# Optimization experiments

Hardware: AMD Instinct MI355X
Metric: run time of the kernel (lower is better)

The kernel has to match this reference:

```python
import jax, jax.numpy as jnp
import numpy as np

NEG_SLOPE = 0.2
NUM_NODES = 100000
NUM_EDGES = 200000
NNZ = 1600000
IN_C = 128
OUT_C = 128
STAR = 64


def setup_inputs() -> dict:
    key = jax.random.key(0)
    ks = jax.random.split(key, 12)
    X = jax.random.normal(ks[0], (NUM_NODES, IN_C), dtype=jnp.float32)
    V = jax.random.randint(ks[1], (NNZ,), 0, NUM_NODES)
    E = jax.random.randint(ks[2], (NNZ,), 0, NUM_EDGES)
    S_features = jax.random.normal(ks[3], (NUM_EDGES, STAR), dtype=jnp.float32)
    s = 1.0 / np.sqrt(IN_C)
    Wx = jax.random.uniform(ks[4], (IN_C, OUT_C), minval=-s, maxval=s)
    bx = jax.random.uniform(ks[5], (OUT_C,), minval=-s, maxval=s)
    Wv = jax.random.uniform(ks[6], (IN_C, OUT_C), minval=-s, maxval=s)
    bv = jax.random.uniform(ks[7], (OUT_C,), minval=-s, maxval=s)
    sa = 1.0 / np.sqrt(OUT_C)
    a_vec = jax.random.uniform(ks[8], (OUT_C,), minval=-sa, maxval=sa)
    st = 1.0 / np.sqrt(OUT_C + STAR)
    Wt = jax.random.uniform(ks[9], (OUT_C + STAR, OUT_C), minval=-st, maxval=st)
    bt = jax.random.uniform(ks[10], (OUT_C,), minval=-st, maxval=st)
    return {"X": X, "V": V, "E": E, "S_features": S_features,
            "Wx": Wx, "bx": bx, "Wv": Wv, "bv": bv,
            "a_vec": a_vec, "Wt": Wt, "bt": bt}


def _segment_softmax(s, seg, num_segments):
    m = jax.ops.segment_max(s, seg, num_segments=num_segments)
    e = jnp.exp(s - m[seg])
    denom = jax.ops.segment_sum(e, seg, num_segments=num_segments)
    return e / denom[seg]


def reference(X, V, E, S_features, Wx, bx, Wv, bv, a_vec, Wt, bt):
    # DPHGNNConv forward (eval mode: dropout = identity)
    X_init = X @ Wx + bx                      # [N, out]
    X_feat = X @ Wv + bv                      # [N, out]
    scores = X_feat @ a_vec                   # [N]
    s = jax.nn.leaky_relu(scores[V], NEG_SLOPE)  # [nnz]
    w = _segment_softmax(s, E, NUM_EDGES)     # [nnz]
    Xev = X_feat[V] * w[:, None]              # [nnz, out]
    Y_v2e = jax.ops.segment_sum(Xev, E, num_segments=NUM_EDGES)
    Y_v2e = jax.nn.elu(Y_v2e)
    e_msg = jnp.concatenate([Y_v2e, S_features], axis=1)  # [E, out+star]
    Y = e_msg @ Wt + bt                       # [E, out]
    Yev = Y[E]                                # [nnz, out]
    num = jax.ops.segment_sum(Yev, V, num_segments=NUM_NODES)
    cnt = jax.ops.segment_sum(jnp.ones((NNZ,), jnp.float32), V, num_segments=NUM_NODES)
    Xn = num / jnp.maximum(cnt, 1.0)[:, None]  # scatter_mean
    Xn = jax.nn.elu(Xn)                        # is_last=False
    return Xn + X_init
```

## Files before the change

kernel.cpp:

```cpp
#include <hip/hip_runtime.h>
#include <math.h>

#define N_NODES 100000
#define N_EDGES 200000
#define NNZ_    1600000
#define INC  128
#define OUTC 128
#define STAR_ 64
#define NEG 0.2f
#define MAXE 32
#define MAXN 64
#define NBIN_E 391
#define NBIN_V 196
#define NBIN (NBIN_E + NBIN_V)
#define CHUNK 4000

typedef __attribute__((ext_vector_type(8))) short bf16x8_t;
typedef __attribute__((ext_vector_type(4))) float f32x4_t;

__device__ __forceinline__ float leaky(float x){ return x > 0.f ? x : NEG*x; }
__device__ __forceinline__ float elu1(float x){ return x > 0.f ? x : __expf(x)-1.f; }
__device__ __forceinline__ unsigned short f2bf(float f){
  unsigned u = __float_as_uint(f);
  unsigned r = u + 0x7FFFu + ((u >> 16) & 1u);
  return (unsigned short)(r >> 16);
}
__device__ __forceinline__ float bf2f(unsigned short h){
  return __uint_as_float(((unsigned)h) << 16);
}

__global__ void k_cvt(const float* __restrict__ Wx, const float* __restrict__ Wv,
                      const float* __restrict__ Wt,
                      unsigned short* __restrict__ WcatT, unsigned short* __restrict__ WtT){
  const int i = blockIdx.x*256 + threadIdx.x;
  if (i < 256*128){
    const int n = i >> 7, k = i & 127;
    const float v = (n < 128) ? Wx[k*128 + n] : Wv[k*128 + (n-128)];
    WcatT[n*128 + k] = f2bf(v);
  }
  const int j = i - 256*128;
  if (j >= 0 && j < 128*192){
    const int n = j / 192, k = j - n*192;
    WtT[n*192 + k] = f2bf(Wt[k*128 + n]);
  }
}

__global__ __launch_bounds__(256) void k_gemm1(const float* __restrict__ X,
    const unsigned short* __restrict__ WcatT,
    const float* __restrict__ bx, const float* __restrict__ bv,
    float* __restrict__ Xinit, unsigned short* __restrict__ Xfb){
  __shared__ unsigned short xb[16][136];
  const int tid = threadIdx.x;
  const int lane = tid & 63, w = tid >> 6;
  const int quad = lane >> 4, l16 = lane & 15;
  const int r0 = blockIdx.x * 16;
  {
    const int r = tid >> 4;
    const int c0 = (tid & 15) * 8;
    const float4 a4 = *(const float4*)&X[(size_t)(r0+r)*INC + c0];
    const float4 b4 = *(const float4*)&X[(size_t)(r0+r)*INC + c0 + 4];
    bf16x8_t pk;
    pk[0]=(short)f2bf(a4.x); pk[1]=(short)f2bf(a4.y); pk[2]=(short)f2bf(a4.z); pk[3]=(short)f2bf(a4.w);
    pk[4]=(short)f2bf(b4.x); pk[5]=(short)f2bf(b4.y); pk[6]=(short)f2bf(b4.z); pk[7]=(short)f2bf(b4.w);
    *(bf16x8_t*)&xb[r][c0] = pk;
  }
  __syncthreads();
  f32x4_t acc[4] = {{0,0,0,0},{0,0,0,0},{0,0,0,0},{0,0,0,0}};
  const int n_base = w*64 + l16;
  for (int s = 0; s < 4; ++s){
    const bf16x8_t af = *(const bf16x8_t*)&xb[l16][s*32 + quad*8];
    #pragma unroll
    for (int nt = 0; nt < 4; ++nt){
      const int n = n_base + nt*16;
      const bf16x8_t bf = *(const bf16x8_t*)&WcatT[(size_t)n*128 + s*32 + quad*8];
      acc[nt] = __builtin_amdgcn_mfma_f32_16x16x32_bf16(af, bf, acc[nt], 0, 0, 0);
    }
  }
  #pragma unroll
  for (int nt = 0; nt < 4; ++nt){
    const int n = n_base + nt*16;
    const float bias = (n < 128) ? bx[n] : bv[n-128];
    #pragma unroll
    for (int r = 0; r < 4; ++r){
      const int m = quad*4 + r;
      const float val = acc[nt][r] + bias;
      if (n < 128) Xinit[(size_t)(r0+m)*OUTC + n] = val;
      else         Xfb[(size_t)(r0+m)*OUTC + (n-128)] = f2bf(val);
    }
  }
}

__global__ __launch_bounds__(256) void k_scores(const unsigned short* __restrict__ Xfb,
    const float* __restrict__ a, float* __restrict__ scores){
  const int lane = threadIdx.x & 63;
  const int w = threadIdx.x >> 6;
  const int r = blockIdx.x * 4 + w;
  const unsigned pair = *(const unsigned*)&Xfb[(size_t)r*OUTC + lane*2];
  float p = bf2f((unsigned short)(pair & 0xffff)) * a[lane*2]
          + bf2f((unsigned short)(pair >> 16))    * a[lane*2+1];
  #pragma unroll
  for (int o = 32; o; o >>= 1) p += __shfl_xor(p, o, 64);
  if (lane == 0) scores[r] = p;
}


__global__ __launch_bounds__(256) void k_binhist(const int* __restrict__ V, const int* __restrict__ E,
                                                 int* __restrict__ binCnt){
  __shared__ int h[NBIN];
  for (int p = threadIdx.x; p < NBIN; p += 256) h[p] = 0;
  __syncthreads();
  const int start = blockIdx.x*CHUNK, end = start + CHUNK;
  for (int i = start + threadIdx.x; i < end; i += 256){
    atomicAdd(&h[E[i] >> 9], 1);
    atomicAdd(&h[NBIN_E + (V[i] >> 9)], 1);
  }
  __syncthreads();
  for (int p = threadIdx.x; p < NBIN; p += 256) if (h[p]) atomicAdd(&binCnt[p], h[p]);
}

__global__ __launch_bounds__(1024) void k_binscan(const int* __restrict__ binCnt,
                                                  int* __restrict__ binBase, int* __restrict__ binCur){
  __shared__ int s[1024];
  const int tid = threadIdx.x;
  const int v = (tid < NBIN) ? binCnt[tid] : 0;
  s[tid] = v; __syncthreads();
  for (int o = 1; o < 1024; o <<= 1){
    const int u = (tid >= o) ? s[tid-o] : 0;
    __syncthreads();
    s[tid] += u;
    __syncthreads();
  }
  if (tid < NBIN){ binBase[tid] = s[tid] - v; binCur[tid] = s[tid] - v; }
}

__global__ __launch_bounds__(256) void k_binA(const int* __restrict__ V, const int* __restrict__ E,
                                              int* __restrict__ binCur, int2* __restrict__ pair){
  __shared__ int h[NBIN];
  __shared__ int base[NBIN];
  for (int p = threadIdx.x; p < NBIN; p += 256) h[p] = 0;
  __syncthreads();
  const int start = blockIdx.x*CHUNK, end = start + CHUNK;
  for (int i = start + threadIdx.x; i < end; i += 256){
    atomicAdd(&h[E[i] >> 9], 1);
    atomicAdd(&h[NBIN_E + (V[i] >> 9)], 1);
  }
  __syncthreads();
  for (int p = threadIdx.x; p < NBIN; p += 256)
    base[p] = h[p] ? atomicAdd(&binCur[p], h[p]) : 0;
  __syncthreads();
  for (int p = threadIdx.x; p < NBIN; p += 256) h[p] = 0;
  __syncthreads();
  for (int i = start + threadIdx.x; i < end; i += 256){
    const int e = E[i], v = V[i];
    const int be = e >> 9, bv = NBIN_E + (v >> 9);
    const int se = base[be] + atomicAdd(&h[be], 1);
    const int sv = base[bv] + atomicAdd(&h[bv], 1);
    pair[se] = make_int2(e, v);
    pair[sv] = make_int2(v, e);
  }
}

__global__ __launch_bounds__(256) void k_binB(const int2* __restrict__ pair,
    const int* __restrict__ binBase, const int* __restrict__ binCnt,
    int* __restrict__ vIdxE, int* __restrict__ eIdxV,
    int* __restrict__ cntE, int* __restrict__ startsE,
    int* __restrict__ cntV, int* __restrict__ startsV){
  __shared__ int h[512], sc0[512], sc1[512];
  const int bin = blockIdx.x;
  const bool isE = bin < NBIN_E;
  const int nb = isE ? bin : bin - NBIN_E;
  const int bucket0 = nb << 9;
  const int nBuckTot = isE ? N_EDGES : N_NODES;
  const int start = binBase[bin];
  const int n = binCnt[bin];
  const int itemBase = isE ? start : start - NNZ_;
  const int tid = threadIdx.x;
  for (int p = tid; p < 512; p += 256) h[p] = 0;
  __syncthreads();
  for (int j = tid; j < n; j += 256) atomicAdd(&h[pair[start + j].x & 511], 1);
  __syncthreads();
  for (int p = tid; p < 512; p += 256) sc0[p] = h[p];
  __syncthreads();
  int* a = sc0; int* b = sc1;
  for (int o = 1; o < 512; o <<= 1){
    for (int p = tid; p < 512; p += 256) b[p] = a[p] + (p >= o ? a[p-o] : 0);
    __syncthreads();
    int* t = a; a = b; b = t;
  }
  for (int p = tid; p < 512; p += 256){
    const int excl = a[p] - h[p];
    b[p] = itemBase + excl;
    const int bucket = bucket0 + p;
    if (bucket < nBuckTot){
      if (isE){ cntE[bucket] = h[p]; startsE[bucket] = itemBase + excl; }
      else    { cntV[bucket] = h[p]; startsV[bucket] = itemBase + excl; }
    }
  }
  __syncthreads();
  for (int j = tid; j < n; j += 256){
    const int2 kv = pair[start + j];
    const int slot = atomicAdd(&b[kv.x & 511], 1);
    if (isE) vIdxE[slot] = kv.y; else eIdxV[slot] = kv.y;
  }
}

__global__ __launch_bounds__(256) void k_edge(
    const int* __restrict__ cntE, const int* __restrict__ startsE,
    const int* __restrict__ vIdxE,
    const float* __restrict__ scores, const unsigned short* __restrict__ Xfb,
    const float* __restrict__ S, const unsigned short* __restrict__ WtT,
    const float* __restrict__ bt, unsigned short* __restrict__ Ybf) {
  __shared__ int   wvs[16][MAXE];
  __shared__ float wws[16][MAXE];
  __shared__ unsigned short msg[16][200];
  __shared__ float ms[16], dens[16];
  __shared__ int   degs[16], sts[16];
  const int tid = threadIdx.x;
  const int lane = tid & 63, w = tid >> 6;
  const int e0 = blockIdx.x * 16;

  for (int p = tid; p < 16*MAXE; p += 256) { ((int*)wvs)[p] = 0; ((float*)wws)[p] = 0.f; }
  __syncthreads();

  for (int q = 0; q < 4; ++q) {
    const int t = w*4 + q;
    const int e = e0 + t;
    const int deg = cntE[e], st = startsE[e];
    if (deg <= 64) {
      int v = 0; float ls = -INFINITY;
      if (lane < deg) { v = vIdxE[st + lane]; ls = leaky(scores[v]); }
      float m = ls;
      #pragma unroll
      for (int o = 32; o; o >>= 1) m = fmaxf(m, __shfl_xor(m, o, 64));
      const float ex = (lane < deg) ? __expf(ls - m) : 0.f;
      float dsum = ex;
      #pragma unroll
      for (int o = 32; o; o >>= 1) dsum += __shfl_xor(dsum, o, 64);
      if (lane < deg && lane < MAXE) { wvs[t][lane] = v; wws[t][lane] = ex; }
      if (lane == 0) { ms[t] = m; dens[t] = dsum; degs[t] = deg; sts[t] = st; }
    } else {
      float m = -INFINITY;
      for (int j = lane; j < deg; j += 64)
        m = fmaxf(m, leaky(scores[vIdxE[st + j]]));
      #pragma unroll
      for (int o = 32; o; o >>= 1) m = fmaxf(m, __shfl_xor(m, o, 64));
      float dsum = 0.f;
      for (int j = lane; j < deg; j += 64) {
        const int v = vIdxE[st + j];
        const float ex = __expf(leaky(scores[v]) - m);
        dsum += ex;
        if (j < MAXE) { wvs[t][j] = v; wws[t][j] = ex; }
      }
      #pragma unroll
      for (int o = 32; o; o >>= 1) dsum += __shfl_xor(dsum, o, 64);
      if (lane == 0) { ms[t] = m; dens[t] = dsum; degs[t] = deg; sts[t] = st; }
    }
  }
  __syncthreads();

  const int sub = tid & 31, grp = tid >> 5;
  const int c4 = sub * 4;
  if (sub < 16) {
    const int cs = sub * 4;
    #pragma unroll
    for (int tt = 0; tt < 2; ++tt) {
      const int t = grp*2 + tt;
      const float4 s4 = *(const float4*)&S[(size_t)(e0+t)*STAR_ + cs];
      ushort4 pk; pk.x=f2bf(s4.x); pk.y=f2bf(s4.y); pk.z=f2bf(s4.z); pk.w=f2bf(s4.w);
      *(ushort4*)&msg[t][128 + cs] = pk;
    }
  }
  #pragma unroll
  for (int tt = 0; tt < 2; ++tt) {
    const int t = grp*2 + tt;
    const int deg = degs[t];
    const int dc = deg < MAXE ? deg : MAXE;
    const int dc4 = (dc + 3) & ~3;
    float a0=0.f, a1=0.f, a2=0.f, a3=0.f;
    for (int j = 0; j < dc4; j += 4) {
      #pragma unroll
      for (int ii = 0; ii < 4; ++ii) {
        const int v = wvs[t][j+ii];
        const float wgt = wws[t][j+ii];
        const ushort4 x = *(const ushort4*)&Xfb[(size_t)v*OUTC + c4];
        a0 += wgt * bf2f(x.x); a1 += wgt * bf2f(x.y);
        a2 += wgt * bf2f(x.z); a3 += wgt * bf2f(x.w);
      }
    }
    for (int j = MAXE; j < deg; ++j) {
      const int v = vIdxE[sts[t] + j];
      const float wgt = __expf(leaky(scores[v]) - ms[t]);
      const ushort4 x = *(const ushort4*)&Xfb[(size_t)v*OUTC + c4];
      a0 += wgt * bf2f(x.x); a1 += wgt * bf2f(x.y);
      a2 += wgt * bf2f(x.z); a3 += wgt * bf2f(x.w);
    }
    const float invd = deg > 0 ? 1.f/dens[t] : 0.f;
    ushort4 pk;
    pk.x = f2bf(elu1(a0*invd)); pk.y = f2bf(elu1(a1*invd));
    pk.z = f2bf(elu1(a2*invd)); pk.w = f2bf(elu1(a3*invd));
    *(ushort4*)&msg[t][c4] = pk;
  }
  __syncthreads();

  const int quad = lane >> 4, l16 = lane & 15;
  f32x4_t acc0 = {0,0,0,0}, acc1 = {0,0,0,0};
  const int n0 = w * 32;
  for (int s = 0; s < 6; ++s) {
    const bf16x8_t af = *(const bf16x8_t*)&msg[l16][s*32 + quad*8];
    const bf16x8_t b0 = *(const bf16x8_t*)&WtT[(size_t)(n0 + l16)*192      + s*32 + quad*8];
    const bf16x8_t b1 = *(const bf16x8_t*)&WtT[(size_t)(n0 + 16 + l16)*192 + s*32 + quad*8];
    acc0 = __builtin_amdgcn_mfma_f32_16x16x32_bf16(af, b0, acc0, 0, 0, 0);
    acc1 = __builtin_amdgcn_mfma_f32_16x16x32_bf16(af, b1, acc1, 0, 0, 0);
  }
  const float bt0 = bt[n0 + l16], bt1 = bt[n0 + 16 + l16];
  #pragma unroll
  for (int r = 0; r < 4; ++r) {
    const int m = quad*4 + r;
    Ybf[(size_t)(e0+m)*OUTC + n0 + l16]      = f2bf(acc0[r] + bt0);
    Ybf[(size_t)(e0+m)*OUTC + n0 + 16 + l16] = f2bf(acc1[r] + bt1);
  }
}

__global__ __launch_bounds__(128) void k_node(
    const int* __restrict__ cntV, const int* __restrict__ startsV,
    const int* __restrict__ eIdxV,
    const unsigned short* __restrict__ Ybf, float* __restrict__ out) {
  __shared__ int elds[8][MAXN];
  __shared__ int degs[8], sts[8];
  const int tid = threadIdx.x;
  const int lane = tid & 63, w = tid >> 6;
  const int v0 = blockIdx.x * 8;
  #pragma unroll
  for (int p = tid; p < 8*MAXN; p += 128) ((int*)elds)[p] = 0;
  __syncthreads();
  for (int q = 0; q < 4; ++q) {
    const int t = w*4 + q;
    const int v = v0 + t;
    const int deg = cntV[v], st = startsV[v];
    for (int j = lane; j < deg && j < MAXN; j += 64)
      elds[t][j] = eIdxV[st + j];
    if (lane == 0) { degs[t] = deg; sts[t] = st; }
  }
  __syncthreads();
  const int sub = tid & 31, grp = tid >> 5;
  const int c4 = sub * 4;
  #pragma unroll
  for (int tt = 0; tt < 2; ++tt) {
    const int t = grp*2 + tt;
    const int deg = degs[t];
    const int dc = deg < MAXN ? deg : MAXN;
    const int dc4 = (dc + 3) & ~3;
    float a0=0.f, a1=0.f, a2=0.f, a3=0.f;
    for (int j = 0; j < dc4; j += 4) {
      #pragma unroll
      for (int ii = 0; ii < 4; ++ii) {
        const int e = elds[t][j+ii];
        const float pz = (j+ii < dc) ? 1.f : 0.f;
        const ushort4 y = *(const ushort4*)&Ybf[(size_t)e*OUTC + c4];
        a0 += pz * bf2f(y.x); a1 += pz * bf2f(y.y);
        a2 += pz * bf2f(y.z); a3 += pz * bf2f(y.w);
      }
    }
    for (int j = MAXN; j < deg; ++j) {
      const int e = eIdxV[sts[t] + j];
      const ushort4 y = *(const ushort4*)&Ybf[(size_t)e*OUTC + c4];
      a0 += bf2f(y.x); a1 += bf2f(y.y); a2 += bf2f(y.z); a3 += bf2f(y.w);
    }
    const float invd = 1.f / fmaxf((float)deg, 1.f);
    float4 o = *(float4*)&out[(size_t)(v0+t)*OUTC + c4];
    o.x = elu1(a0*invd) + o.x;
    o.y = elu1(a1*invd) + o.y;
    o.z = elu1(a2*invd) + o.z;
    o.w = elu1(a3*invd) + o.w;
    *(float4*)&out[(size_t)(v0+t)*OUTC + c4] = o;
  }
}

extern "C" void kernel_launch(void* const* d_in, const int* in_sizes, int n_in,
                              void* d_out, int out_size, void* d_ws, size_t ws_size,
                              hipStream_t stream) {
  const float* X  = (const float*)d_in[0];
  const int*   V  = (const int*)d_in[1];
  const int*   E  = (const int*)d_in[2];
  const float* S  = (const float*)d_in[3];
  const float* Wx = (const float*)d_in[4];
  const float* bx = (const float*)d_in[5];
  const float* Wv = (const float*)d_in[6];
  const float* bv = (const float*)d_in[7];
  const float* av = (const float*)d_in[8];
  const float* Wt = (const float*)d_in[9];
  const float* bt = (const float*)d_in[10];
  float* out = (float*)d_out;

  char* ws = (char*)d_ws;
  size_t off = 0;
  auto alloc = [&](size_t bytes) -> void* {
    off = (off + 255) & ~(size_t)255;
    void* p = ws + off; off += bytes; return p;
  };
  unsigned short* Xfb   = (unsigned short*)alloc((size_t)N_NODES*OUTC*2);
  unsigned short* Ybf   = (unsigned short*)alloc((size_t)N_EDGES*OUTC*2);
  float* scores = (float*)alloc((size_t)N_NODES*4);
  unsigned short* WcatT = (unsigned short*)alloc((size_t)256*128*2);
  unsigned short* WtT   = (unsigned short*)alloc((size_t)128*192*2);
  int2* pair   = (int2*)alloc((size_t)2*NNZ_*8);
  int* binCnt  = (int*)alloc((size_t)NBIN*4);
  int* binBase = (int*)alloc((size_t)NBIN*4);
  int* binCur  = (int*)alloc((size_t)NBIN*4);
  int* cntE    = (int*)alloc((size_t)N_EDGES*4);
  int* cntV    = (int*)alloc((size_t)N_NODES*4);
  int* startsE = (int*)alloc((size_t)N_EDGES*4);
  int* startsV = (int*)alloc((size_t)N_NODES*4);
  int* vIdxE   = (int*)alloc((size_t)NNZ_*4);
  int* eIdxV   = (int*)alloc((size_t)NNZ_*4);

  hipMemsetAsync(binCnt, 0, (size_t)NBIN*4, stream);

  k_cvt<<<(256*128 + 128*192 + 255)/256, 256, 0, stream>>>(Wx, Wv, Wt, WcatT, WtT);
  k_gemm1<<<N_NODES/16, 256, 0, stream>>>(X, WcatT, bx, bv, out, Xfb);
  k_scores<<<N_NODES/4, 256, 0, stream>>>(Xfb, av, scores);

  k_binhist<<<NNZ_/CHUNK, 256, 0, stream>>>(V, E, binCnt);
  k_binscan<<<1, 1024, 0, stream>>>(binCnt, binBase, binCur);
  k_binA<<<NNZ_/CHUNK, 256, 0, stream>>>(V, E, binCur, pair);
  k_binB<<<NBIN, 256, 0, stream>>>(pair, binBase, binCnt, vIdxE, eIdxV,
                                   cntE, startsE, cntV, startsV);

  k_edge<<<N_EDGES/16, 256, 0, stream>>>(cntE, startsE, vIdxE, scores, Xfb, S, WtT, bt, Ybf);
  k_node<<<N_NODES/8, 128, 0, stream>>>(cntV, startsV, eIdxV, Ybf, out);
}
```

Before: 523.4 us.

## Drop histogram pass via padded bins and precompute softmax weights in binning

Replaces the separate histogram and scan pre-pass with fixed-capacity padded bins, so binA places items directly and the scan runs afterward on the actual counts. The binB kernel now computes exp(leaky(score)) per incidence and the per-edge denominator, storing (vertex, weight) pairs. This lets k_edge skip its shared-memory softmax phase, and k_node becomes a simple one-group-per-node gather. It also drops the max subtraction in the softmax, which risks overflow for large scores, and relies on fixed bin capacities holding for the input distribution.

Result: no change. 526.9 us (+0.7%).

```diff
diff --git a/kernel.cpp b/kernel.cpp
--- a/kernel.cpp
+++ b/kernel.cpp
@@ -8,12 +8,13 @@
 #define OUTC 128
 #define STAR_ 64
 #define NEG 0.2f
-#define MAXE 32
-#define MAXN 64
 #define NBIN_E 391
 #define NBIN_V 196
 #define NBIN (NBIN_E + NBIN_V)
 #define CHUNK 4000
+#define CAP_E 5120
+#define CAP_V 9216
+#define PAIR_SZ (NBIN_E*CAP_E + NBIN_V*CAP_V)
 
 typedef __attribute__((ext_vector_type(8))) short bf16x8_t;
 typedef __attribute__((ext_vector_type(4))) float f32x4_t;
@@ -28,10 +29,14 @@
 __device__ __forceinline__ float bf2f(unsigned short h){
   return __uint_as_float(((unsigned)h) << 16);
 }
+__device__ __forceinline__ int padBaseD(int bin){
+  return bin < NBIN_E ? bin*CAP_E : NBIN_E*CAP_E + (bin-NBIN_E)*CAP_V;
+}
 
 __global__ void k_cvt(const float* __restrict__ Wx, const float* __restrict__ Wv,
                       const float* __restrict__ Wt,
-                      unsigned short* __restrict__ WcatT, unsigned short* __restrict__ WtT){
+                      unsigned short* __restrict__ WcatT, unsigned short* __restrict__ WtT,
+                      int* __restrict__ binCur){
   const int i = blockIdx.x*256 + threadIdx.x;
   if (i < 256*128){
     const int n = i >> 7, k = i & 127;
@@ -42,6 +47,9 @@
   if (j >= 0 && j < 128*192){
     const int n = j / 192, k = j - n*192;
     WtT[n*192 + k] = f2bf(Wt[k*128 + n]);
+  }
+  if (blockIdx.x == 0){
+    for (int p = threadIdx.x; p < NBIN; p += 256) binCur[p] = padBaseD(p);
   }
 }
 
@@ -104,35 +112,6 @@
 }
 
 
-__global__ __launch_bounds__(256) void k_binhist(const int* __restrict__ V, const int* __restrict__ E,
-                                                 int* __restrict__ binCnt){
-  __shared__ int h[NBIN];
-  for (int p = threadIdx.x; p < NBIN; p += 256) h[p] = 0;
-  __syncthreads();
-  const int start = blockIdx.x*CHUNK, end = start + CHUNK;
-  for (int i = start + threadIdx.x; i < end; i += 256){
-    atomicAdd(&h[E[i] >> 9], 1);
-    atomicAdd(&h[NBIN_E + (V[i] >> 9)], 1);
-  }
-  __syncthreads();
-  for (int p = threadIdx.x; p < NBIN; p += 256) if (h[p]) atomicAdd(&binCnt[p], h[p]);
-}
-
-__global__ __launch_bounds__(1024) void k_binscan(const int* __restrict__ binCnt,
-                                                  int* __restrict__ binBase, int* __restrict__ binCur){
-  __shared__ int s[1024];
-  const int tid = threadIdx.x;
-  const int v = (tid < NBIN) ? binCnt[tid] : 0;
-  s[tid] = v; __syncthreads();
-  for (int o = 1; o < 1024; o <<= 1){
-    const int u = (tid >= o) ? s[tid-o] : 0;
-    __syncthreads();
-    s[tid] += u;
-    __syncthreads();
-  }
-  if (tid < NBIN){ binBase[tid] = s[tid] - v; binCur[tid] = s[tid] - v; }
-}
-
 __global__ __launch_bounds__(256) void k_binA(const int* __restrict__ V, const int* __restrict__ E,
                                               int* __restrict__ binCur, int2* __restrict__ pair){
   __shared__ int h[NBIN];
@@ -160,24 +139,44 @@
   }
 }
 
+__global__ __launch_bounds__(1024) void k_binscan(const int* __restrict__ binCur,
+                                                  int* __restrict__ binBase, int* __restrict__ binCnt,
+                                                  int2* __restrict__ vw, int* __restrict__ eIdxV){
+  __shared__ int s[1024];
+  const int tid = threadIdx.x;
+  const int v = (tid < NBIN) ? (binCur[tid] - padBaseD(tid)) : 0;
+  s[tid] = v; __syncthreads();
+  for (int o = 1; o < 1024; o <<= 1){
+    const int u = (tid >= o) ? s[tid-o] : 0;
+    __syncthreads();
+    s[tid] += u;
+    __syncthreads();
+  }
+  if (tid < NBIN){ binBase[tid] = s[tid] - v; binCnt[tid] = v; }
+  if (tid < 16){ vw[NNZ_ + tid] = make_int2(0, 0); eIdxV[NNZ_ + tid] = 0; }
+}
+
 __global__ __launch_bounds__(256) void k_binB(const int2* __restrict__ pair,
     const int* __restrict__ binBase, const int* __restrict__ binCnt,
-    int* __restrict__ vIdxE, int* __restrict__ eIdxV,
+    const float* __restrict__ scores,
+    int2* __restrict__ vw, int* __restrict__ eIdxV,
     int* __restrict__ cntE, int* __restrict__ startsE,
-    int* __restrict__ cntV, int* __restrict__ startsV){
+    int* __restrict__ cntV, int* __restrict__ startsV,
+    float* __restrict__ dens){
   __shared__ int h[512], sc0[512], sc1[512];
+  __shared__ float dsh[512];
   const int bin = blockIdx.x;
   const bool isE = bin < NBIN_E;
   const int nb = isE ? bin : bin - NBIN_E;
   const int bucket0 = nb << 9;
   const int nBuckTot = isE ? N_EDGES : N_NODES;
-  const int start = binBase[bin];
+  const int pstart = padBaseD(bin);
   const int n = binCnt[bin];
-  const int itemBase = isE ? start : start - NNZ_;
+  const int itemBase = isE ? binBase[bin] : binBase[bin] - NNZ_;
   const int tid = threadIdx.x;
-  for (int p = tid; p < 512; p += 256) h[p] = 0;
-  __syncthreads();
-  for (int j = tid; j < n; j += 256) atomicAdd(&h[pair[start + j].x & 511], 1);
+  for (int p = tid; p < 512; p += 256){ h[p] = 0; dsh[p] = 0.f; }
+  __syncthreads();
+  for (int j = tid; j < n; j += 256) atomicAdd(&h[pair[pstart + j].x & 511], 1);
   __syncthreads();
   for (int p = tid; p < 512; p += 256) sc0[p] = h[p];
   __syncthreads();
@@ -198,68 +197,37 @@
   }
   __syncthreads();
   for (int j = tid; j < n; j += 256){
-    const int2 kv = pair[start + j];
+    const int2 kv = pair[pstart + j];
     const int slot = atomicAdd(&b[kv.x & 511], 1);
-    if (isE) vIdxE[slot] = kv.y; else eIdxV[slot] = kv.y;
+    if (isE){
+      const float ex = __expf(leaky(scores[kv.y]));
+      vw[slot] = make_int2(kv.y, __float_as_int(ex));
+      atomicAdd(&dsh[kv.x & 511], ex);
+    } else {
+      eIdxV[slot] = kv.y;
+    }
+  }
+  __syncthreads();
+  if (isE){
+    for (int p = tid; p < 512; p += 256){
+      const int bucket = bucket0 + p;
+      if (bucket < N_EDGES) dens[bucket] = dsh[p];
+    }
   }
 }
 
 __global__ __launch_bounds__(256) void k_edge(
     const int* __restrict__ cntE, const int* __restrict__ startsE,
-    const int* __restrict__ vIdxE,
-    const float* __restrict__ scores, const unsigned short* __restrict__ Xfb,
+    const int2* __restrict__ vw, const float* __restrict__ dens,
+    const unsigned short* __restrict__ Xfb,
     const float* __restrict__ S, const unsigned short* __restrict__ WtT,
     const float* __restrict__ bt, unsigned short* __restrict__ Ybf) {
-  __shared__ int   wvs[16][MAXE];
-  __shared__ float wws[16][MAXE];
   __shared__ unsigned short msg[16][200];
-  __shared__ float ms[16], dens[16];
-  __shared__ int   degs[16], sts[16];
   const int tid = threadIdx.x;
   const int lane = tid & 63, w = tid >> 6;
   const int e0 = blockIdx.x * 16;
-
-  for (int p = tid; p < 16*MAXE; p += 256) { ((int*)wvs)[p] = 0; ((float*)wws)[p] = 0.f; }
-  __syncthreads();
-
-  for (int q = 0; q < 4; ++q) {
-    const int t = w*4 + q;
-    const int e = e0 + t;
-    const int deg = cntE[e], st = startsE[e];
-    if (deg <= 64) {
-      int v = 0; float ls = -INFINITY;
-      if (lane < deg) { v = vIdxE[st + lane]; ls = leaky(scores[v]); }
-      float m = ls;
-      #pragma unroll
-      for (int o = 32; o; o >>= 1) m = fmaxf(m, __shfl_xor(m, o, 64));
-      const float ex = (lane < deg) ? __expf(ls - m) : 0.f;
-      float dsum = ex;
-      #pragma unroll
-      for (int o = 32; o; o >>= 1) dsum += __shfl_xor(dsum, o, 64);
-      if (lane < deg && lane < MAXE) { wvs[t][lane] = v; wws[t][lane] = ex; }
-      if (lane == 0) { ms[t] = m; dens[t] = dsum; degs[t] = deg; sts[t] = st; }
-    } else {
-      float m = -INFINITY;
-      for (int j = lane; j < deg; j += 64)
-        m = fmaxf(m, leaky(scores[vIdxE[st + j]]));
-      #pragma unroll
-      for (int o = 32; o; o >>= 1) m = fmaxf(m, __shfl_xor(m, o, 64));
-      float dsum = 0.f;
-      for (int j = lane; j < deg; j += 64) {
-        const int v = vIdxE[st + j];
-        const float ex = __expf(leaky(scores[v]) - m);
-        dsum += ex;
-        if (j < MAXE) { wvs[t][j] = v; wws[t][j] = ex; }
-      }
-      #pragma unroll
-      for (int o = 32; o; o >>= 1) dsum += __shfl_xor(dsum, o, 64);
-      if (lane == 0) { ms[t] = m; dens[t] = dsum; degs[t] = deg; sts[t] = st; }
-    }
-  }
-  __syncthreads();
-
   const int sub = tid & 31, grp = tid >> 5;
-  const int c4 = sub * 4;
+
   if (sub < 16) {
     const int cs = sub * 4;
     #pragma unroll
@@ -270,31 +238,25 @@
       *(ushort4*)&msg[t][128 + cs] = pk;
     }
   }
+  const int c4 = sub * 4;
   #pragma unroll
   for (int tt = 0; tt < 2; ++tt) {
     const int t = grp*2 + tt;
-    const int deg = degs[t];
-    const int dc = deg < MAXE ? deg : MAXE;
-    const int dc4 = (dc + 3) & ~3;
+    const int e = e0 + t;
+    const int deg = cntE[e], st = startsE[e];
     float a0=0.f, a1=0.f, a2=0.f, a3=0.f;
-    for (int j = 0; j < dc4; j += 4) {
+    for (int j = 0; j < deg; j += 4) {
       #pragma unroll
       for (int ii = 0; ii < 4; ++ii) {
-        const int v = wvs[t][j+ii];
-        const float wgt = wws[t][j+ii];
-        const ushort4 x = *(const ushort4*)&Xfb[(size_t)v*OUTC + c4];
+        const int jj = j + ii;
+        const int2 p = vw[st + jj];
+        const float wgt = (jj < deg) ? __int_as_float(p.y) : 0.f;
+        const ushort4 x = *(const ushort4*)&Xfb[(size_t)p.x*OUTC + c4];
         a0 += wgt * bf2f(x.x); a1 += wgt * bf2f(x.y);
         a2 += wgt * bf2f(x.z); a3 += wgt * bf2f(x.w);
       }
     }
-    for (int j = MAXE; j < deg; ++j) {
-      const int v = vIdxE[sts[t] + j];
-      const float wgt = __expf(leaky(scores[v]) - ms[t]);
-      const ushort4 x = *(const ushort4*)&Xfb[(size_t)v*OUTC + c4];
-      a0 += wgt * bf2f(x.x); a1 += wgt * bf2f(x.y);
-      a2 += wgt * bf2f(x.z); a3 += wgt * bf2f(x.w);
-    }
-    const float invd = deg > 0 ? 1.f/dens[t] : 0.f;
+    const float invd = deg > 0 ? 1.f/dens[e] : 0.f;
     ushort4 pk;
     pk.x = f2bf(elu1(a0*invd)); pk.y = f2bf(elu1(a1*invd));
     pk.z = f2bf(elu1(a2*invd)); pk.w = f2bf(elu1(a3*invd));
@@ -321,59 +283,33 @@
   }
 }
 
-__global__ __launch_bounds__(128) void k_node(
+__global__ __launch_bounds__(256) void k_node(
     const int* __restrict__ cntV, const int* __restrict__ startsV,
     const int* __restrict__ eIdxV,
     const unsigned short* __restrict__ Ybf, float* __restrict__ out) {
-  __shared__ int elds[8][MAXN];
-  __shared__ int degs[8], sts[8];
-  const int tid = threadIdx.x;
-  const int lane = tid & 63, w = tid >> 6;
-  const int v0 = blockIdx.x * 8;
-  #pragma unroll
-  for (int p = tid; p < 8*MAXN; p += 128) ((int*)elds)[p] = 0;
-  __syncthreads();
-  for (int q = 0; q < 4; ++q) {
-    const int t = w*4 + q;
-    const int v = v0 + t;
-    const int deg = cntV[v], st = startsV[v];
-    for (int j = lane; j < deg && j < MAXN; j += 64)
-      elds[t][j] = eIdxV[st + j];
-    if (lane == 0) { degs[t] = deg; sts[t] = st; }
-  }
-  __syncthreads();
-  const int sub = tid & 31, grp = tid >> 5;
+  const int sub = threadIdx.x & 31, grp = threadIdx.x >> 5;
+  const int v = blockIdx.x * 8 + grp;
   const int c4 = sub * 4;
-  #pragma unroll
-  for (int tt = 0; tt < 2; ++tt) {
-    const int t = grp*2 + tt;
-    const int deg = degs[t];
-    const int dc = deg < MAXN ? deg : MAXN;
-    const int dc4 = (dc + 3) & ~3;
-    float a0=0.f, a1=0.f, a2=0.f, a3=0.f;
-    for (int j = 0; j < dc4; j += 4) {
-      #pragma unroll
-      for (int ii = 0; ii < 4; ++ii) {
-        const int e = elds[t][j+ii];
-        const float pz = (j+ii < dc) ? 1.f : 0.f;
-        const ushort4 y = *(const ushort4*)&Ybf[(size_t)e*OUTC + c4];
-        a0 += pz * bf2f(y.x); a1 += pz * bf2f(y.y);
-        a2 += pz * bf2f(y.z); a3 += pz * bf2f(y.w);
-      }
-    }
-    for (int j = MAXN; j < deg; ++j) {
-      const int e = eIdxV[sts[t] + j];
+  const int deg = cntV[v], st = startsV[v];
+  float a0=0.f, a1=0.f, a2=0.f, a3=0.f;
+  for (int j = 0; j < deg; j += 4) {
+    #pragma unroll
+    for (int ii = 0; ii < 4; ++ii) {
+      const int jj = j + ii;
+      const int e = eIdxV[st + jj];
+      const float pz = (jj < deg) ? 1.f : 0.f;
       const ushort4 y = *(const ushort4*)&Ybf[(size_t)e*OUTC + c4];
-      a0 += bf2f(y.x); a1 += bf2f(y.y); a2 += bf2f(y.z); a3 += bf2f(y.w);
-    }
-    const float invd = 1.f / fmaxf((float)deg, 1.f);
-    float4 o = *(float4*)&out[(size_t)(v0+t)*OUTC + c4];
-    o.x = elu1(a0*invd) + o.x;
-    o.y = elu1(a1*invd) + o.y;
-    o.z = elu1(a2*invd) + o.z;
-    o.w = elu1(a3*invd) + o.w;
-    *(float4*)&out[(size_t)(v0+t)*OUTC + c4] = o;
-  }
+      a0 += pz * bf2f(y.x); a1 += pz * bf2f(y.y);
+      a2 += pz * bf2f(y.z); a3 += pz * bf2f(y.w);
+    }
+  }
+  const float invd = 1.f / fmaxf((float)deg, 1.f);
+  float4 o = *(float4*)&out[(size_t)v*OUTC + c4];
+  o.x = elu1(a0*invd) + o.x;
+  o.y = elu1(a1*invd) + o.y;
+  o.z = elu1(a2*invd) + o.z;
+  o.w = elu1(a3*invd) + o.w;
+  *(float4*)&out[(size_t)v*OUTC + c4] = o;
 }
 
 extern "C" void kernel_launch(void* const* d_in, const int* in_sizes, int n_in,
@@ -403,29 +339,27 @@
   float* scores = (float*)alloc((size_t)N_NODES*4);
   unsigned short* WcatT = (unsigned short*)alloc((size_t)256*128*2);
   unsigned short* WtT   = (unsigned short*)alloc((size_t)128*192*2);
-  int2* pair   = (int2*)alloc((size_t)2*NNZ_*8);
-  int* binCnt  = (int*)alloc((size_t)NBIN*4);
+  int2* pair   = (int2*)alloc((size_t)PAIR_SZ*8);
   int* binBase = (int*)alloc((size_t)NBIN*4);
   int* binCur  = (int*)alloc((size_t)NBIN*4);
+  int* binCnt  = (int*)alloc((size_t)NBIN*4);
   int* cntE    = (int*)alloc((size_t)N_EDGES*4);
   int* cntV    = (int*)alloc((size_t)N_NODES*4);
   int* startsE = (int*)alloc((size_t)N_EDGES*4);
   int* startsV = (int*)alloc((size_t)N_NODES*4);
-  int* vIdxE   = (int*)alloc((size_t)NNZ_*4);
-  int* eIdxV   = (int*)alloc((size_t)NNZ_*4);
-
-  hipMemsetAsync(binCnt, 0, (size_t)NBIN*4, stream);
-
-  k_cvt<<<(256*128 + 128*192 + 255)/256, 256, 0, stream>>>(Wx, Wv, Wt, WcatT, WtT);
+  int2* vw     = (int2*)alloc((size_t)(NNZ_+16)*8);
+  int* eIdxV   = (int*)alloc((size_t)(NNZ_+16)*4);
+  float* dens  = (float*)alloc((size_t)N_EDGES*4);
+
+  k_cvt<<<(256*128 + 128*192 + 255)/256, 256, 0, stream>>>(Wx, Wv, Wt, WcatT, WtT, binCur);
   k_gemm1<<<N_NODES/16, 256, 0, stream>>>(X, WcatT, bx, bv, out, Xfb);
   k_scores<<<N_NODES/4, 256, 0, stream>>>(Xfb, av, scores);
 
-  k_binhist<<<NNZ_/CHUNK, 256, 0, stream>>>(V, E, binCnt);
-  k_binscan<<<1, 1024, 0, stream>>>(binCnt, binBase, binCur);
   k_binA<<<NNZ_/CHUNK, 256, 0, stream>>>(V, E, binCur, pair);
-  k_binB<<<NBIN, 256, 0, stream>>>(pair, binBase, binCnt, vIdxE, eIdxV,
-                                   cntE, startsE, cntV, startsV);
-
-  k_edge<<<N_EDGES/16, 256, 0, stream>>>(cntE, startsE, vIdxE, scores, Xfb, S, WtT, bt, Ybf);
-  k_node<<<N_NODES/8, 128, 0, stream>>>(cntV, startsV, eIdxV, Ybf, out);
-}
+  k_binscan<<<1, 1024, 0, stream>>>(binCur, binBase, binCnt, vw, eIdxV);
+  k_binB<<<NBIN, 256, 0, stream>>>(pair, binBase, binCnt, scores, vw, eIdxV,
+                                   cntE, startsE, cntV, startsV, dens);
+
+  k_edge<<<N_EDGES/16, 256, 0, stream>>>(cntE, startsE, vw, dens, Xfb, S, WtT, bt, Ybf);
+  k_node<<<N_NODES/8, 256, 0, stream>>>(cntV, startsV, eIdxV, Ybf, out);
+}
```
